# Optimization experiments

Hardware: AMD Instinct MI355X
Metric: run time of the kernel (lower is better)

The kernel has to match this reference:

```python
import jax, jax.numpy as jnp
import numpy as np
import math

B, S, H = 2, 2048, 2048
NH, HD = 32, 64
BASE, SCALE = 10000.0, 2.0
MAX_POS, ORIG_MAX_POS = 8192, 8192
BETA_FAST, BETA_SLOW = 32, 1
EPS = 1e-6


def _yarn_cos_sin():
    # revised_yarn: scale inv_freq by 1/((1-mask)*scale + mask)
    inv_freq = 1.0 / BASE ** (np.arange(0, HD, 2, dtype=np.float64) / HD)
    def corr(nr):
        return HD * math.log(ORIG_MAX_POS / (nr * 2 * math.pi)) / (2 * math.log(BASE))
    low = max(math.floor(corr(BETA_FAST)), 0)
    high = min(math.ceil(corr(BETA_SLOW)), HD - 1)
    hi = high + 0.001 if low == high else high
    ramp = np.clip((np.arange(HD // 2, dtype=np.float64) - low) / (hi - low), 0.0, 1.0)
    mask = 1.0 - ramp  # extrapolation_factor = 1
    inv_freq = inv_freq / ((1.0 - mask) * SCALE + mask)
    mscale = (0.1 * math.log(SCALE) + 1.0) if SCALE > 1 else 1.0
    t = np.arange(MAX_POS, dtype=np.float64)
    freqs = np.outer(t, inv_freq)
    emb = np.concatenate([freqs, freqs], axis=-1)
    return np.cos(emb) * mscale, np.sin(emb) * mscale

_COS_NP, _SIN_NP = _yarn_cos_sin()


def rotate_half(x):
    x1, x2 = jnp.split(x, 2, axis=-1)
    return jnp.concatenate([-x2, x1], axis=-1)


def rms_norm(x, w):
    v = jnp.mean(jnp.square(x.astype(jnp.float32)), axis=-1, keepdims=True)
    return (x.astype(jnp.float32) * jax.lax.rsqrt(v + EPS)).astype(x.dtype) * w


def localized_filtering(x, lf1, lf2, w1, b1, w2, b2, ln_w):
    # x: (B,S,H); torch works in (B,H,S,1) with kernel-(2,1) convs over seq
    residual = x
    xi = jnp.transpose(x, (0, 2, 1))[:, :, :, None]  # (B,H,S,1)
    xi = jnp.concatenate([lf1, xi], axis=2)          # (B,H,S+1,1)
    dn = ('NCHW', 'OIHW', 'NCHW')
    o1 = jax.lax.conv_general_dilated(xi, w1, (1, 1), 'VALID', dimension_numbers=dn)
    o1 = o1 + b1[None, :, None, None]                # (B,H/2,S,1)
    o1c = jnp.concatenate([lf2, o1], axis=2)         # (B,H/2,S+1,1)
    o2 = jax.lax.conv_general_dilated(o1c, w2, (1, 1), 'VALID', dimension_numbers=dn)
    o2 = o2 + b2[None, :, None, None]                # (B,H,S,1)
    o2 = jnp.transpose(o2[:, :, :, 0], (0, 2, 1))    # (B,S,H)
    return rms_norm(o2 + residual, ln_w)


def setup_inputs():
    key = jax.random.key(0)
    ks = jax.random.split(key, 8)
    f = lambda k, shp: jax.random.normal(k, shp, dtype=jnp.float32) * 0.02
    return {
        'hidden_states': jax.random.normal(ks[0], (B, S, H), dtype=jnp.float32),
        'position_ids': jnp.broadcast_to(jnp.arange(S, dtype=jnp.int32)[None, :], (B, S)),
        'lf1_cache': jnp.zeros((B, H, 1, 1), jnp.float32),
        'lf2_cache': jnp.zeros((B, H // 2, 1, 1), jnp.float32),
        'Wqk': f(ks[1], (2 * H, H)),
        'Wv': f(ks[2], (H, H)),
        'Wo': f(ks[3], (H, H)),
        'conv1_w': f(ks[4], (H // 2, H, 2, 1)),
        'conv1_b': jnp.zeros((H // 2,), jnp.float32),
        'conv2_w': f(ks[5], (H, H // 2, 2, 1)),
        'conv2_b': jnp.zeros((H,), jnp.float32),
        'ln_w': jnp.ones((H,), jnp.float32),
    }


def reference(hidden_states, position_ids, lf1_cache, lf2_cache, Wqk, Wv, Wo,
              conv1_w, conv1_b, conv2_w, conv2_b, ln_w):
    cos = jnp.asarray(_COS_NP, jnp.float32)
    sin = jnp.asarray(_SIN_NP, jnp.float32)
    # v from raw hidden states
    v = (hidden_states @ Wv.T).reshape(B, S, NH, HD).transpose(0, 2, 1, 3)  # (B,NH,S,HD)
    # localized filtering gate feeds q/k projection
    lf = localized_filtering(hidden_states, lf1_cache, lf2_cache,
                             conv1_w, conv1_b, conv2_w, conv2_b, ln_w)
    qk = (lf @ Wqk.T).reshape(B, S, NH, 2 * HD)  # per-head [q|k] split
    q = qk[..., :HD].transpose(0, 2, 1, 3)       # (B,NH,S,HD)
    k = qk[..., HD:].transpose(0, 2, 1, 3)
    cos_p = cos[position_ids][:, None, :, :]     # (B,1,S,HD)
    sin_p = sin[position_ids][:, None, :, :]
    q = q * cos_p + rotate_half(q) * sin_p
    k = k * cos_p + rotate_half(k) * sin_p
    scores = jnp.einsum('bhqd,bhkd->bhqk', q, k) / math.sqrt(HD)
    causal = jnp.tril(jnp.ones((S, S), dtype=bool))
    scores = jnp.where(causal[None, None], scores, jnp.finfo(scores.dtype).min)
    attn = jax.nn.softmax(scores, axis=-1)
    ctx = jnp.einsum('bhqk,bhkd->bhqd', attn, v)
    out = ctx.transpose(0, 2, 1, 3).reshape(B, S, H) @ Wo.T
    return out
```

## Files before the change

kernel.cpp:

```cpp
#include <hip/hip_runtime.h>
#include <hip/hip_bf16.h>
#include <math.h>
#include <stdint.h>

typedef __hip_bfloat16 bf16;
using f32x4 = __attribute__((ext_vector_type(4))) float;
using s16x8 = __attribute__((ext_vector_type(8))) short;

constexpr int Bc = 2, Sc = 2048, Hc = 2048, NHc = 32, HDc = 64;
constexpr int Mc = Bc * Sc;
constexpr int MAXPOS = 8192;

constexpr size_t OFF_WV  = 0;
constexpr size_t OFF_WQK = OFF_WV  + (size_t)Hc * Hc * 2;
constexpr size_t OFF_WO  = OFF_WQK + (size_t)2 * Hc * Hc * 2;
constexpr size_t OFF_W1  = OFF_WO  + (size_t)Hc * Hc * 2;
constexpr size_t OFF_W2  = OFF_W1  + (size_t)(Hc/2) * (2*Hc) * 2;
constexpr size_t OFF_HS  = OFF_W2  + (size_t)Hc * Hc * 2;
constexpr size_t OFF_XPR = OFF_HS  + (size_t)Mc * Hc * 2;
constexpr size_t OFF_O1  = OFF_XPR + (size_t)Mc * Hc * 2;
constexpr size_t OFF_O1P = OFF_O1  + (size_t)Mc * (Hc/2) * 2;
constexpr size_t OFF_O2  = OFF_O1P + (size_t)Mc * (Hc/2) * 2;
constexpr size_t OFF_LF  = OFF_O2  + (size_t)Mc * Hc * 4;
constexpr size_t OFF_VT  = OFF_LF  + (size_t)Mc * Hc * 2;
constexpr size_t OFF_COS = OFF_VT  + (size_t)Mc * Hc * 2;
constexpr size_t OFF_SIN = OFF_COS + (size_t)MAXPOS * HDc * 4;
constexpr size_t OFF_Q   = OFF_XPR;
constexpr size_t OFF_K   = OFF_HS;
constexpr size_t OFF_CTX = OFF_O1;

__device__ __forceinline__ f32x4 mfma16(s16x8 a, s16x8 b, f32x4 c) {
  return __builtin_amdgcn_mfma_f32_16x16x32_bf16(a, b, c, 0, 0, 0);
}
__device__ __forceinline__ void gload16(const bf16* g, bf16* l) {
  __builtin_amdgcn_global_load_lds(
      (__attribute__((address_space(1))) void*)g,
      (__attribute__((address_space(3))) void*)l, 16, 0, 0);
}
__device__ __forceinline__ uint16_t bfbits(float x) {
  union { bf16 h; uint16_t u; } v; v.h = __float2bfloat16(x); return v.u;
}
__device__ __forceinline__ uint32_t pkbf(float a, float b) {
  return (uint32_t)bfbits(a) | ((uint32_t)bfbits(b) << 16);
}
__device__ __forceinline__ void block_bar() {
  asm volatile("" ::: "memory");
  __builtin_amdgcn_s_barrier();
  asm volatile("" ::: "memory");
}
template <int N> __device__ __forceinline__ void vm_wait() {
  if constexpr (N == 0)      asm volatile("s_waitcnt vmcnt(0)" ::: "memory");
  else if constexpr (N == 3) asm volatile("s_waitcnt vmcnt(3)" ::: "memory");
  else if constexpr (N == 4) asm volatile("s_waitcnt vmcnt(4)" ::: "memory");
  else if constexpr (N == 6) asm volatile("s_waitcnt vmcnt(6)" ::: "memory");
  else if constexpr (N == 8) asm volatile("s_waitcnt vmcnt(8)" ::: "memory");
}

__global__ void k_cvt(const float* __restrict__ in, bf16* __restrict__ out, int n) {
  int i = blockIdx.x * 256 + threadIdx.x;
  if (i < n) out[i] = __float2bfloat16(in[i]);
}

__global__ void k_cvt_hs(const float* __restrict__ hs, const float* __restrict__ lf1,
                         bf16* __restrict__ hsb, bf16* __restrict__ xprev) {
  int i = blockIdx.x * 256 + threadIdx.x;
  if (i >= Mc * Hc) return;
  float v = hs[i];
  bf16 b = __float2bfloat16(v);
  hsb[i] = b;
  int row = i >> 11, col = i & (Hc - 1);
  int s = row & (Sc - 1), bb = row >> 11;
  if (s + 1 < Sc) xprev[i + Hc] = b;
  if (s == 0)     xprev[i] = __float2bfloat16(lf1[bb * Hc + col]);
}

__global__ void k_repack1(const float* __restrict__ w, bf16* __restrict__ out) {
  int i = blockIdx.x * 256 + threadIdx.x;
  if (i >= (Hc/2) * 2 * Hc) return;
  int oc = i >> 12, k = i & 4095;
  int ic = k & (Hc - 1), t = k >> 11;
  out[i] = __float2bfloat16(w[((size_t)oc * Hc + ic) * 2 + t]);
}
__global__ void k_repack2(const float* __restrict__ w, bf16* __restrict__ out) {
  int i = blockIdx.x * 256 + threadIdx.x;
  if (i >= Hc * Hc) return;
  int c = i >> 11, k = i & (Hc - 1);
  int oc = k & (Hc/2 - 1), t = k >> 10;
  out[i] = __float2bfloat16(w[((size_t)c * (Hc/2) + oc) * 2 + t]);
}

__global__ void k_prefill_o1p(const float* __restrict__ lf2, bf16* __restrict__ o1p) {
  int i = blockIdx.x * 256 + threadIdx.x;
  if (i >= Bc * (Hc/2)) return;
  int b = i >> 10, n = i & (Hc/2 - 1);
  o1p[(size_t)b * Sc * (Hc/2) + n] = __float2bfloat16(lf2[i]);
}

struct InvF { double v[32]; double mscale; };

__global__ void k_costab(InvF f, float* __restrict__ ct, float* __restrict__ st) {
  int i = blockIdx.x * 256 + threadIdx.x;
  if (i >= MAXPOS * HDc) return;
  int p = i >> 6, d = i & 63;
  double ang = (double)p * f.v[d & 31];
  ct[i] = (float)(cos(ang) * f.mscale);
  st[i] = (float)(sin(ang) * f.mscale);
}

__global__ __launch_bounds__(256) void k_rmsnorm(const float* __restrict__ x,
                                                 const float* __restrict__ w,
                                                 bf16* __restrict__ out) {
  __shared__ float red[4];
  int row = blockIdx.x;
  const float* xr = x + (size_t)row * Hc;
  float ss = 0.f;
  for (int c = threadIdx.x; c < Hc; c += 256) { float v = xr[c]; ss += v * v; }
  for (int off = 32; off; off >>= 1) ss += __shfl_down(ss, off, 64);
  if ((threadIdx.x & 63) == 0) red[threadIdx.x >> 6] = ss;
  __syncthreads();
  float sc = rsqrtf((red[0] + red[1] + red[2] + red[3]) / Hc + 1e-6f);
  for (int c = threadIdx.x; c < Hc; c += 256)
    out[(size_t)row * Hc + c] = __float2bfloat16(xr[c] * sc * w[c]);
}

template <int EPI, int BM = 128>
__global__ __launch_bounds__(256) void gemm_bt(
    const bf16* __restrict__ A0, const bf16* __restrict__ A1, int Ksplit,
    const bf16* __restrict__ Bw, int K, int N, void* __restrict__ Cout,
    const float* __restrict__ bias, const float* __restrict__ resid,
    bf16* __restrict__ aux) {
  constexpr int MR = BM / 32;
  __shared__ __align__(16) bf16 As[2][BM * 32];
  __shared__ __align__(16) bf16 Bs[2][128 * 32];
  const int tid = threadIdx.x;
  const int bm = blockIdx.y, bn = blockIdx.x;
  const int w = tid >> 6, l = tid & 63;
  const int wm = (w >> 1) * (BM / 2), wn = (w & 1) * 64;
  const int lrow = l & 15, lg = l >> 4, lk = lg * 8;
  const int r0 = tid >> 2, cofs = (tid & 3) * 8;

  auto stage = [&](int buf, int kt) {
    const int kcol = kt * 32;
    const bf16* Au; int kc;
    if (kcol < Ksplit) { Au = A0; kc = kcol; } else { Au = A1; kc = kcol - Ksplit; }
    gload16(Au + (size_t)(bm * BM + r0) * Ksplit + kc + cofs,        &As[buf][tid * 8]);
    if constexpr (BM == 128)
      gload16(Au + (size_t)(bm * BM + r0 + 64) * Ksplit + kc + cofs, &As[buf][2048 + tid * 8]);
    gload16(Bw + (size_t)(bn * 128 + r0) * K + kcol + cofs,          &Bs[buf][tid * 8]);
    gload16(Bw + (size_t)(bn * 128 + r0 + 64) * K + kcol + cofs,     &Bs[buf][2048 + tid * 8]);
  };

  f32x4 acc[MR][4] = {};
  const int nkt = K / 32;
  stage(0, 0);
  __syncthreads();
  for (int kt = 0; kt < nkt; ++kt) {
    const int cur = kt & 1;
    if (kt + 1 < nkt) stage(cur ^ 1, kt + 1);
    s16x8 af[MR], bfr[4];
#pragma unroll
    for (int m = 0; m < MR; ++m)
      af[m] = *(const s16x8*)&As[cur][(wm + m * 16 + lrow) * 32 + lk];
#pragma unroll
    for (int n = 0; n < 4; ++n)
      bfr[n] = *(const s16x8*)&Bs[cur][(wn + n * 16 + lrow) * 32 + lk];
    __builtin_amdgcn_s_setprio(1);
#pragma unroll
    for (int m = 0; m < MR; ++m)
#pragma unroll
      for (int n = 0; n < 4; ++n)
        acc[m][n] = mfma16(af[m], bfr[n], acc[m][n]);
    __builtin_amdgcn_s_setprio(0);
    __syncthreads();
  }
#pragma unroll
  for (int m = 0; m < MR; ++m)
#pragma unroll
    for (int n = 0; n < 4; ++n)
#pragma unroll
      for (int r = 0; r < 4; ++r) {
        const int grow = bm * BM + wm + m * 16 + lg * 4 + r;
        const int gcol = bn * 128 + wn + n * 16 + lrow;
        float v = acc[m][n][r];
        if constexpr (EPI == 1) {
          v += bias[gcol];
          bf16 bv = __float2bfloat16(v);
          ((bf16*)Cout)[(size_t)grow * N + gcol] = bv;
          if ((grow & (Sc - 1)) != Sc - 1) aux[(size_t)(grow + 1) * N + gcol] = bv;
        } else {
          ((float*)Cout)[(size_t)grow * N + gcol] = v;
        }
      }
}

template <int EPI, int BN>
__global__ __launch_bounds__(512, 2) void gemm8(
    const bf16* __restrict__ A0, const bf16* __restrict__ A1, int Ksplit,
    const bf16* __restrict__ Bw, int K, int N, void* __restrict__ Cout,
    const float* __restrict__ bias, const float* __restrict__ resid,
    const int* __restrict__ pos, const float* __restrict__ ct,
    const float* __restrict__ st, bf16* __restrict__ out2) {
  constexpr int BM = 256;
  constexpr int L = (BN == 256) ? 4 : 3;
  constexpr int TILE = (BM + BN) * 32;
  constexpr int MR = (BN == 256) ? 8 : 4;
  __shared__ __align__(16) bf16 lds[3][TILE];
  const int tid = threadIdx.x;
  const int w = tid >> 6, l = tid & 63;
  const int lrow = l & 15, lg = l >> 4;
  const int wm = (BN == 256) ? (w >> 2) * 128 : (w & 3) * 64;
  const int wn = (BN == 256) ? (w & 3) * 64 : (w >> 2) * 64;
  const int gx = gridDim.x;
  const int lin = blockIdx.y * gx + blockIdx.x;
  const int cx = gx >> 2, cy = gridDim.y >> 1;
  const int c = lin & 7, idx = lin >> 3;
  const int bn = (c & 3) * cx + idx % cx;
  const int bm = (c >> 2) * cy + idx / cx;

  auto ld1 = [&](const bf16* srcbase, size_t stride, bf16* ldst, int ci) {
    const int pr = ci >> 3, rem = ci & 7;
    const int r = pr * 2 + (rem >> 2), g = (rem & 3) ^ (pr & 3);
    gload16(srcbase + (size_t)r * stride + g * 8, ldst + ci * 8);
  };
  auto stage = [&](int kt, int slot) {
    const int kcol = kt * 32;
    const bf16* Au; int kc;
    if (kcol < Ksplit) { Au = A0; kc = kcol; } else { Au = A1; kc = kcol - Ksplit; }
    const bf16* As_ = Au + (size_t)bm * BM * Ksplit + kc;
    bf16* ldsA = lds[slot];
    ld1(As_, Ksplit, ldsA, tid);
    ld1(As_, Ksplit, ldsA, tid + 512);
    const bf16* Bs_ = Bw + (size_t)bn * BN * K + kcol;
    bf16* ldsB = lds[slot] + BM * 32;
    ld1(Bs_, K, ldsB, tid);
    if constexpr (BN == 256) ld1(Bs_, K, ldsB, tid + 512);
  };
  auto frag = [&](const bf16* base, int r) -> s16x8 {
    const int s = ((r >> 1) << 3) + ((r & 1) << 2) + (lg ^ ((r >> 1) & 3));
    return *(const s16x8*)(base + s * 8);
  };

  f32x4 acc[MR][4] = {};
  const int nkt = K / 32;
  stage(0, 0);
  stage(1, 1);
  for (int t = 0; t < nkt; ++t) {
    if (t + 2 < nkt) { stage(t + 2, (t + 2) % 3); vm_wait<2 * L>(); }
    else if (t + 1 < nkt) { vm_wait<L>(); }
    else { vm_wait<0>(); }
    block_bar();
    const bf16* Asl = lds[t % 3];
    const bf16* Bsl = Asl + BM * 32;
    s16x8 af[MR], bfr[4];
#pragma unroll
    for (int m = 0; m < MR; ++m) af[m] = frag(Asl, wm + m * 16 + lrow);
#pragma unroll
    for (int n = 0; n < 4; ++n) bfr[n] = frag(Bsl, wn + n * 16 + lrow);
    __builtin_amdgcn_s_setprio(1);
#pragma unroll
    for (int m = 0; m < MR; ++m)
#pragma unroll
      for (int n = 0; n < 4; ++n)
        acc[m][n] = mfma16(af[m], bfr[n], acc[m][n]);
    __builtin_amdgcn_s_setprio(0);
    block_bar();
  }
  if constexpr (EPI == 6) {
    const int gcol0 = bn * BN + wn;
    const int h = gcol0 >> 7, half = (gcol0 >> 6) & 1;
    bf16* outp = half ? out2 : (bf16*)Cout;
    const float qsc = half ? 1.0f : 0.125f * 1.44269504088896f;
#pragma unroll
    for (int m = 0; m < MR; ++m)
#pragma unroll
      for (int r = 0; r < 4; ++r) {
        const int grow = bm * BM + wm + m * 16 + lg * 4 + r;
        const int p = pos[grow];
        const int bb = grow >> 11, s = grow & (Sc - 1);
        bf16* rowp = outp + ((size_t)(bb * NHc + h) * Sc + s) * 64;
#pragma unroll
        for (int n = 0; n < 2; ++n) {
          const int dd = n * 16 + lrow;
          const float c0 = ct[p * 64 + dd],      s0 = st[p * 64 + dd];
          const float c1 = ct[p * 64 + 32 + dd], s1 = st[p * 64 + 32 + dd];
          const float v0 = acc[m][n][r], v1 = acc[m][n + 2][r];
          rowp[dd]      = __float2bfloat16((v0 * c0 - v1 * s0) * qsc);
          rowp[dd + 32] = __float2bfloat16((v1 * c1 + v0 * s1) * qsc);
        }
      }
  } else {
#pragma unroll
    for (int m = 0; m < MR; ++m)
#pragma unroll
      for (int n = 0; n < 4; ++n)
#pragma unroll
        for (int r = 0; r < 4; ++r) {
          const int grow = bm * BM + wm + m * 16 + lg * 4 + r;
          const int gcol = bn * BN + wn + n * 16 + lrow;
          float v = acc[m][n][r];
          if constexpr (EPI == 2) {
            v += bias[gcol] + resid[(size_t)grow * N + gcol];
            ((float*)Cout)[(size_t)grow * N + gcol] = v;
          } else if constexpr (EPI == 5) {
            const int b = gcol >> 11, s = gcol & (Sc - 1);
            ((bf16*)Cout)[((size_t)(b * Hc + grow)) * Sc + s] = __float2bfloat16(v);
          } else {
            ((float*)Cout)[(size_t)grow * N + gcol] = v;
          }
        }
  }
}

__global__ __launch_bounds__(256) void k_attn(const bf16* __restrict__ Q,
                                              const bf16* __restrict__ Kg,
                                              const bf16* __restrict__ Vt,
                                              bf16* __restrict__ ctx) {
  __shared__ __align__(16) bf16 Ks[2][64 * 64];
  __shared__ __align__(16) bf16 Vs[2][64 * 64];
  __shared__ __align__(16) uint32_t Pl[4][2][2][16][20];
  const int tid = threadIdx.x;
  const int w = tid >> 6, l = tid & 63;
  const int lrow = l & 15, lg = l >> 4, lk = lg * 8;
  const int bh = blockIdx.x;
  const int tile = blockIdx.y;
  const bf16* Qp = Q  + (size_t)bh * Sc * HDc;
  const bf16* Kp = Kg + (size_t)bh * Sc * HDc;
  const bf16* Vp = Vt + (size_t)bh * HDc * Sc;
  const int b = bh >> 5, h = bh & 31;
  const s16x8 ones8 = {16256, 16256, 16256, 16256, 16256, 16256, 16256, 16256};

  const int srow0 = tid >> 3, schunk = tid & 7;

  for (int pass = 0; pass < 2; ++pass) {
    const int base = (pass == 0) ? tile * 128 : (Sc - 128 - tile * 128);
    const int q0 = base + w * 32;
    const int NT = base / 64 + 2;

    s16x8 qa[2][2];
#pragma unroll
    for (int m = 0; m < 2; ++m)
#pragma unroll
      for (int hf = 0; hf < 2; ++hf)
        qa[m][hf] = *(const s16x8*)&Qp[(size_t)(q0 + m * 16 + lrow) * 64 + hf * 32 + lk];

    f32x4 o[2][4] = {};
    f32x4 lsf[2] = {};
    float mx[2] = {-1e30f, -1e30f};

    {
      gload16(Kp + (size_t)srow0 * 64 + ((schunk ^ (srow0 & 7)) << 3), &Ks[0][tid * 8]);
      gload16(Kp + (size_t)(32 + srow0) * 64 + ((schunk ^ ((32 + srow0) & 7)) << 3),
              &Ks[0][2048 + tid * 8]);
      gload16(Vp + (size_t)srow0 * Sc + ((schunk ^ (srow0 & 7)) << 3), &Vs[0][tid * 8]);
      gload16(Vp + (size_t)(32 + srow0) * Sc + ((schunk ^ ((32 + srow0) & 7)) << 3),
              &Vs[0][2048 + tid * 8]);
    }
    __syncthreads();

    for (int t = 0; t < NT; ++t) {
      const int cur = t & 1;
      const int kv0 = t * 64;
      if (t + 1 < NT) {
        const int nkv = kv0 + 64;
        const int nb = cur ^ 1;
        gload16(Kp + (size_t)(nkv + srow0) * 64 + ((schunk ^ (srow0 & 7)) << 3),
                &Ks[nb][tid * 8]);
        gload16(Kp + (size_t)(nkv + 32 + srow0) * 64 + ((schunk ^ ((32 + srow0) & 7)) << 3),
                &Ks[nb][2048 + tid * 8]);
        gload16(Vp + (size_t)srow0 * Sc + nkv + ((schunk ^ (srow0 & 7)) << 3),
                &Vs[nb][tid * 8]);
        gload16(Vp + (size_t)(32 + srow0) * Sc + nkv + ((schunk ^ ((32 + srow0) & 7)) << 3),
                &Vs[nb][2048 + tid * 8]);
      }
      if (kv0 <= q0) {
        s16x8 kc[8], vc[4][2];
#pragma unroll
        for (int c = 0; c < 4; ++c)
#pragma unroll
          for (int hf = 0; hf < 2; ++hf) {
            const int row = c * 16 + lrow;
            kc[c * 2 + hf] =
                *(const s16x8*)&Ks[cur][row * 64 + (((hf << 2) + lg) ^ (row & 7)) * 8];
          }
#pragma unroll
        for (int db = 0; db < 4; ++db)
#pragma unroll
          for (int kh = 0; kh < 2; ++kh) {
            const int row = db * 16 + lrow;
            vc[db][kh] =
                *(const s16x8*)&Vs[cur][row * 64 + (((kh << 2) + lg) ^ (row & 7)) * 8];
          }
        const bool lastit = (kv0 + 64 > q0);

#pragma unroll
        for (int m = 0; m < 2; ++m) {
          f32x4 s[4];
          __builtin_amdgcn_s_setprio(1);
#pragma unroll
          for (int c = 0; c < 4; ++c) {
            f32x4 z = {};
            z = mfma16(kc[c * 2], qa[m][0], z);
            z = mfma16(kc[c * 2 + 1], qa[m][1], z);
            s[c] = z;
          }
          __builtin_amdgcn_s_setprio(0);

          if (lastit) {
            const int qq = q0 + m * 16 + lrow;
#pragma unroll
            for (int c = 0; c < 4; ++c)
#pragma unroll
              for (int r = 0; r < 4; ++r)
                if (kv0 + c * 16 + lg * 4 + r > qq) s[c][r] = -1e30f;
          }
          float t16 = fmaxf(
              fmaxf(fmaxf(fmaxf(s[0][0], s[0][1]), fmaxf(s[0][2], s[0][3])),
                    fmaxf(fmaxf(s[1][0], s[1][1]), fmaxf(s[1][2], s[1][3]))),
              fmaxf(fmaxf(fmaxf(s[2][0], s[2][1]), fmaxf(s[2][2], s[2][3])),
                    fmaxf(fmaxf(s[3][0], s[3][1]), fmaxf(s[3][2], s[3][3]))));
          if (!__all(t16 <= mx[m] + 8.0f)) {
            t16 = fmaxf(t16, __shfl_xor(t16, 16, 64));
            t16 = fmaxf(t16, __shfl_xor(t16, 32, 64));
            const float mnew = fmaxf(mx[m], t16);
            const float sold = __builtin_amdgcn_exp2f(mx[m] - mnew);
            mx[m] = mnew;
            lsf[m] *= sold;
#pragma unroll
            for (int db = 0; db < 4; ++db) o[m][db] *= sold;
          }
          float p[4][4];
#pragma unroll
          for (int c = 0; c < 4; ++c)
#pragma unroll
            for (int r = 0; r < 4; ++r)
              p[c][r] = __builtin_amdgcn_exp2f(s[c][r] - mx[m]);
#pragma unroll
          for (int kh = 0; kh < 2; ++kh) {
            *(uint64_t*)&Pl[w][m][kh][lrow][lg * 2] =
                (uint64_t)pkbf(p[kh * 2][0], p[kh * 2][1]) |
                ((uint64_t)pkbf(p[kh * 2][2], p[kh * 2][3]) << 32);
            *(uint64_t*)&Pl[w][m][kh][lrow][8 + lg * 2] =
                (uint64_t)pkbf(p[kh * 2 + 1][0], p[kh * 2 + 1][1]) |
                ((uint64_t)pkbf(p[kh * 2 + 1][2], p[kh * 2 + 1][3]) << 32);
          }
          const s16x8 pb0 = *(const s16x8*)&Pl[w][m][0][lrow][lg * 4];
          const s16x8 pb1 = *(const s16x8*)&Pl[w][m][1][lrow][lg * 4];
          __builtin_amdgcn_s_setprio(1);
#pragma unroll
          for (int db = 0; db < 4; ++db) o[m][db] = mfma16(vc[db][0], pb0, o[m][db]);
          lsf[m] = mfma16(ones8, pb0, lsf[m]);
#pragma unroll
          for (int db = 0; db < 4; ++db) o[m][db] = mfma16(vc[db][1], pb1, o[m][db]);
          lsf[m] = mfma16(ones8, pb1, lsf[m]);
          __builtin_amdgcn_s_setprio(0);
        }
      }
      __syncthreads();
    }
#pragma unroll
    for (int m = 0; m < 2; ++m) {
      const float inv = 1.0f / lsf[m][0];
      const int qrow = q0 + m * 16 + lrow;
      const size_t rowoff = ((size_t)(b * Sc + qrow)) * Hc + h * 64;
#pragma unroll
      for (int db = 0; db < 4; ++db) {
        uint64_t pk = (uint64_t)bfbits(o[m][db][0] * inv) |
                      ((uint64_t)bfbits(o[m][db][1] * inv) << 16) |
                      ((uint64_t)bfbits(o[m][db][2] * inv) << 32) |
                      ((uint64_t)bfbits(o[m][db][3] * inv) << 48);
        *(uint64_t*)&ctx[rowoff + db * 16 + lg * 4] = pk;
      }
    }
    __syncthreads();
  }
}

extern "C" void kernel_launch(void* const* d_in, const int* in_sizes, int n_in,
                              void* d_out, int out_size, void* d_ws, size_t ws_size,
                              hipStream_t stream) {
  (void)in_sizes; (void)n_in; (void)out_size; (void)ws_size;
  const float* hs  = (const float*)d_in[0];
  const int*   pos = (const int*)d_in[1];
  const float* lf1 = (const float*)d_in[2];
  const float* lf2 = (const float*)d_in[3];
  const float* Wqk = (const float*)d_in[4];
  const float* Wv  = (const float*)d_in[5];
  const float* Wo  = (const float*)d_in[6];
  const float* c1w = (const float*)d_in[7];
  const float* c1b = (const float*)d_in[8];
  const float* c2w = (const float*)d_in[9];
  const float* c2b = (const float*)d_in[10];
  const float* lnw = (const float*)d_in[11];
  float* out = (float*)d_out;
  char*  ws  = (char*)d_ws;

  bf16* wvB   = (bf16*)(ws + OFF_WV);
  bf16* wqkB  = (bf16*)(ws + OFF_WQK);
  bf16* woB   = (bf16*)(ws + OFF_WO);
  bf16* w1B   = (bf16*)(ws + OFF_W1);
  bf16* w2B   = (bf16*)(ws + OFF_W2);
  bf16* hsB   = (bf16*)(ws + OFF_HS);
  bf16* xprB  = (bf16*)(ws + OFF_XPR);
  bf16* o1B   = (bf16*)(ws + OFF_O1);
  bf16* o1pB  = (bf16*)(ws + OFF_O1P);
  float* o2F  = (float*)(ws + OFF_O2);
  bf16* lfB   = (bf16*)(ws + OFF_LF);
  bf16* vtB   = (bf16*)(ws + OFF_VT);
  float* cosT = (float*)(ws + OFF_COS);
  float* sinT = (float*)(ws + OFF_SIN);
  bf16* qB    = (bf16*)(ws + OFF_Q);
  bf16* kB    = (bf16*)(ws + OFF_K);
  bf16* ctxB  = (bf16*)(ws + OFF_CTX);

  InvF f;
  {
    const double base = 10000.0, scale = 2.0;
    const int hd = HDc;
    auto corr = [&](double nr) {
      return hd * log(8192.0 / (nr * 2.0 * M_PI)) / (2.0 * log(base));
    };
    double low = floor(corr(32.0)); if (low < 0) low = 0;
    double high = ceil(corr(1.0));  if (high > hd - 1) high = hd - 1;
    double hi = (low == high) ? high + 0.001 : high;
    for (int i = 0; i < 32; ++i) {
      double inv = 1.0 / pow(base, (2.0 * i) / hd);
      double ramp = ((double)i - low) / (hi - low);
      ramp = ramp < 0.0 ? 0.0 : (ramp > 1.0 ? 1.0 : ramp);
      double mask = 1.0 - ramp;
      f.v[i] = inv / ((1.0 - mask) * scale + mask);
    }
    f.mscale = 0.1 * log(scale) + 1.0;
  }

  k_cvt<<<(Hc * Hc + 255) / 256, 256, 0, stream>>>(Wv, wvB, Hc * Hc);
  k_cvt<<<(2 * Hc * Hc + 255) / 256, 256, 0, stream>>>(Wqk, wqkB, 2 * Hc * Hc);
  k_cvt<<<(Hc * Hc + 255) / 256, 256, 0, stream>>>(Wo, woB, Hc * Hc);
  k_repack1<<<((Hc / 2) * 2 * Hc + 255) / 256, 256, 0, stream>>>(c1w, w1B);
  k_repack2<<<(Hc * Hc + 255) / 256, 256, 0, stream>>>(c2w, w2B);
  k_cvt_hs<<<(Mc * Hc + 255) / 256, 256, 0, stream>>>(hs, lf1, hsB, xprB);
  k_prefill_o1p<<<(Bc * (Hc / 2) + 255) / 256, 256, 0, stream>>>(lf2, o1pB);
  k_costab<<<(MAXPOS * HDc + 255) / 256, 256, 0, stream>>>(f, cosT, sinT);

  gemm_bt<1, 64><<<dim3((Hc / 2) / 128, Mc / 64), 256, 0, stream>>>(
      xprB, hsB, Hc, w1B, 2 * Hc, Hc / 2, o1B, c1b, nullptr, o1pB);
  gemm8<5, 128><<<dim3(Mc / 128, Hc / 256), 512, 0, stream>>>(
      wvB, wvB, Hc, hsB, Hc, Mc, vtB, nullptr, nullptr, nullptr, nullptr, nullptr, nullptr);
  gemm8<2, 128><<<dim3(Hc / 128, Mc / 256), 512, 0, stream>>>(
      o1pB, o1B, Hc / 2, w2B, Hc, Hc, o2F, c2b, hs, nullptr, nullptr, nullptr, nullptr);
  k_rmsnorm<<<Mc, 256, 0, stream>>>(o2F, lnw, lfB);
  gemm8<6, 256><<<dim3((2 * Hc) / 256, Mc / 256), 512, 0, stream>>>(
      lfB, lfB, Hc, wqkB, Hc, 2 * Hc, qB, nullptr, nullptr, pos, cosT, sinT, kB);
  k_attn<<<dim3(64, 8), 256, 0, stream>>>(qB, kB, vtB, ctxB);
  gemm8<4, 128><<<dim3(Hc / 128, Mc / 256), 512, 0, stream>>>(
      ctxB, ctxB, Hc, woB, Hc, Hc, out, nullptr, nullptr, nullptr, nullptr, nullptr, nullptr);
}
```

Baseline: 461.6 us.

## Port conv1 GEMM to gemm8 and split attention passes across 512-thread blocks

The conv1 GEMM moves from the older double-buffered 256-thread gemm_bt kernel to the triple-buffered 512-thread gemm8 kernel with a new 128x128 tile variant and a bias/shifted-copy epilogue. The attention kernel now runs its two causal query passes (early and late tiles) concurrently in two 4-wave halves of a 512-thread block, instead of looping over them one after another. This is meant to balance the causal work within each block and add more waves per block to hide latency. In exchange it adds LDS for the per-wave P buffers and a launch-bounds hint that limits register use.

```diff
diff --git a/kernel.cpp b/kernel.cpp
--- a/kernel.cpp
+++ b/kernel.cpp
@@ -50,6 +50,7 @@
 }
 template <int N> __device__ __forceinline__ void vm_wait() {
   if constexpr (N == 0)      asm volatile("s_waitcnt vmcnt(0)" ::: "memory");
+  else if constexpr (N == 2) asm volatile("s_waitcnt vmcnt(2)" ::: "memory");
   else if constexpr (N == 3) asm volatile("s_waitcnt vmcnt(3)" ::: "memory");
   else if constexpr (N == 4) asm volatile("s_waitcnt vmcnt(4)" ::: "memory");
   else if constexpr (N == 6) asm volatile("s_waitcnt vmcnt(6)" ::: "memory");
@@ -123,93 +124,25 @@
     out[(size_t)row * Hc + c] = __float2bfloat16(xr[c] * sc * w[c]);
 }
 
-template <int EPI, int BM = 128>
-__global__ __launch_bounds__(256) void gemm_bt(
-    const bf16* __restrict__ A0, const bf16* __restrict__ A1, int Ksplit,
-    const bf16* __restrict__ Bw, int K, int N, void* __restrict__ Cout,
-    const float* __restrict__ bias, const float* __restrict__ resid,
-    bf16* __restrict__ aux) {
-  constexpr int MR = BM / 32;
-  __shared__ __align__(16) bf16 As[2][BM * 32];
-  __shared__ __align__(16) bf16 Bs[2][128 * 32];
-  const int tid = threadIdx.x;
-  const int bm = blockIdx.y, bn = blockIdx.x;
-  const int w = tid >> 6, l = tid & 63;
-  const int wm = (w >> 1) * (BM / 2), wn = (w & 1) * 64;
-  const int lrow = l & 15, lg = l >> 4, lk = lg * 8;
-  const int r0 = tid >> 2, cofs = (tid & 3) * 8;
-
-  auto stage = [&](int buf, int kt) {
-    const int kcol = kt * 32;
-    const bf16* Au; int kc;
-    if (kcol < Ksplit) { Au = A0; kc = kcol; } else { Au = A1; kc = kcol - Ksplit; }
-    gload16(Au + (size_t)(bm * BM + r0) * Ksplit + kc + cofs,        &As[buf][tid * 8]);
-    if constexpr (BM == 128)
-      gload16(Au + (size_t)(bm * BM + r0 + 64) * Ksplit + kc + cofs, &As[buf][2048 + tid * 8]);
-    gload16(Bw + (size_t)(bn * 128 + r0) * K + kcol + cofs,          &Bs[buf][tid * 8]);
-    gload16(Bw + (size_t)(bn * 128 + r0 + 64) * K + kcol + cofs,     &Bs[buf][2048 + tid * 8]);
-  };
-
-  f32x4 acc[MR][4] = {};
-  const int nkt = K / 32;
-  stage(0, 0);
-  __syncthreads();
-  for (int kt = 0; kt < nkt; ++kt) {
-    const int cur = kt & 1;
-    if (kt + 1 < nkt) stage(cur ^ 1, kt + 1);
-    s16x8 af[MR], bfr[4];
-#pragma unroll
-    for (int m = 0; m < MR; ++m)
-      af[m] = *(const s16x8*)&As[cur][(wm + m * 16 + lrow) * 32 + lk];
-#pragma unroll
-    for (int n = 0; n < 4; ++n)
-      bfr[n] = *(const s16x8*)&Bs[cur][(wn + n * 16 + lrow) * 32 + lk];
-    __builtin_amdgcn_s_setprio(1);
-#pragma unroll
-    for (int m = 0; m < MR; ++m)
-#pragma unroll
-      for (int n = 0; n < 4; ++n)
-        acc[m][n] = mfma16(af[m], bfr[n], acc[m][n]);
-    __builtin_amdgcn_s_setprio(0);
-    __syncthreads();
-  }
-#pragma unroll
-  for (int m = 0; m < MR; ++m)
-#pragma unroll
-    for (int n = 0; n < 4; ++n)
-#pragma unroll
-      for (int r = 0; r < 4; ++r) {
-        const int grow = bm * BM + wm + m * 16 + lg * 4 + r;
-        const int gcol = bn * 128 + wn + n * 16 + lrow;
-        float v = acc[m][n][r];
-        if constexpr (EPI == 1) {
-          v += bias[gcol];
-          bf16 bv = __float2bfloat16(v);
-          ((bf16*)Cout)[(size_t)grow * N + gcol] = bv;
-          if ((grow & (Sc - 1)) != Sc - 1) aux[(size_t)(grow + 1) * N + gcol] = bv;
-        } else {
-          ((float*)Cout)[(size_t)grow * N + gcol] = v;
-        }
-      }
-}
-
-template <int EPI, int BN>
+template <int EPI, int BM, int BN>
 __global__ __launch_bounds__(512, 2) void gemm8(
     const bf16* __restrict__ A0, const bf16* __restrict__ A1, int Ksplit,
     const bf16* __restrict__ Bw, int K, int N, void* __restrict__ Cout,
     const float* __restrict__ bias, const float* __restrict__ resid,
     const int* __restrict__ pos, const float* __restrict__ ct,
     const float* __restrict__ st, bf16* __restrict__ out2) {
-  constexpr int BM = 256;
-  constexpr int L = (BN == 256) ? 4 : 3;
+  constexpr int L = (BM + BN) / 128;
   constexpr int TILE = (BM + BN) * 32;
-  constexpr int MR = (BN == 256) ? 8 : 4;
+  constexpr int MF = (BM == 256) ? ((BN == 256) ? 8 : 4) : 4;
+  constexpr int NF = (BN == 256) ? 4 : ((BM == 256) ? 4 : 2);
   __shared__ __align__(16) bf16 lds[3][TILE];
   const int tid = threadIdx.x;
   const int w = tid >> 6, l = tid & 63;
   const int lrow = l & 15, lg = l >> 4;
-  const int wm = (BN == 256) ? (w >> 2) * 128 : (w & 3) * 64;
-  const int wn = (BN == 256) ? (w & 3) * 64 : (w >> 2) * 64;
+  const int wm = (BM == 256) ? ((BN == 256) ? (w >> 2) * 128 : (w & 3) * 64)
+                             : (w >> 2) * 64;
+  const int wn = (BM == 256) ? ((BN == 256) ? (w & 3) * 64 : (w >> 2) * 64)
+                             : (w & 3) * 32;
   const int gx = gridDim.x;
   const int lin = blockIdx.y * gx + blockIdx.x;
   const int cx = gx >> 2, cy = gridDim.y >> 1;
@@ -229,7 +162,7 @@
     const bf16* As_ = Au + (size_t)bm * BM * Ksplit + kc;
     bf16* ldsA = lds[slot];
     ld1(As_, Ksplit, ldsA, tid);
-    ld1(As_, Ksplit, ldsA, tid + 512);
+    if constexpr (BM == 256) ld1(As_, Ksplit, ldsA, tid + 512);
     const bf16* Bs_ = Bw + (size_t)bn * BN * K + kcol;
     bf16* ldsB = lds[slot] + BM * 32;
     ld1(Bs_, K, ldsB, tid);
@@ -240,7 +173,7 @@
     return *(const s16x8*)(base + s * 8);
   };
 
-  f32x4 acc[MR][4] = {};
+  f32x4 acc[MF][NF] = {};
   const int nkt = K / 32;
   stage(0, 0);
   stage(1, 1);
@@ -251,16 +184,16 @@
     block_bar();
     const bf16* Asl = lds[t % 3];
     const bf16* Bsl = Asl + BM * 32;
-    s16x8 af[MR], bfr[4];
-#pragma unroll
-    for (int m = 0; m < MR; ++m) af[m] = frag(Asl, wm + m * 16 + lrow);
-#pragma unroll
-    for (int n = 0; n < 4; ++n) bfr[n] = frag(Bsl, wn + n * 16 + lrow);
+    s16x8 af[MF], bfr[NF];
+#pragma unroll
+    for (int m = 0; m < MF; ++m) af[m] = frag(Asl, wm + m * 16 + lrow);
+#pragma unroll
+    for (int n = 0; n < NF; ++n) bfr[n] = frag(Bsl, wn + n * 16 + lrow);
     __builtin_amdgcn_s_setprio(1);
 #pragma unroll
-    for (int m = 0; m < MR; ++m)
-#pragma unroll
-      for (int n = 0; n < 4; ++n)
+    for (int m = 0; m < MF; ++m)
+#pragma unroll
+      for (int n = 0; n < NF; ++n)
         acc[m][n] = mfma16(af[m], bfr[n], acc[m][n]);
     __builtin_amdgcn_s_setprio(0);
     block_bar();
@@ -271,7 +204,7 @@
     bf16* outp = half ? out2 : (bf16*)Cout;
     const float qsc = half ? 1.0f : 0.125f * 1.44269504088896f;
 #pragma unroll
-    for (int m = 0; m < MR; ++m)
+    for (int m = 0; m < MF; ++m)
 #pragma unroll
       for (int r = 0; r < 4; ++r) {
         const int grow = bm * BM + wm + m * 16 + lg * 4 + r;
@@ -290,15 +223,20 @@
       }
   } else {
 #pragma unroll
-    for (int m = 0; m < MR; ++m)
-#pragma unroll
-      for (int n = 0; n < 4; ++n)
+    for (int m = 0; m < MF; ++m)
+#pragma unroll
+      for (int n = 0; n < NF; ++n)
 #pragma unroll
         for (int r = 0; r < 4; ++r) {
           const int grow = bm * BM + wm + m * 16 + lg * 4 + r;
           const int gcol = bn * BN + wn + n * 16 + lrow;
           float v = acc[m][n][r];
-          if constexpr (EPI == 2) {
+          if constexpr (EPI == 1) {
+            v += bias[gcol];
+            bf16 bv = __float2bfloat16(v);
+            ((bf16*)Cout)[(size_t)grow * N + gcol] = bv;
+            if ((grow & (Sc - 1)) != Sc - 1) out2[(size_t)(grow + 1) * N + gcol] = bv;
+          } else if constexpr (EPI == 2) {
             v += bias[gcol] + resid[(size_t)grow * N + gcol];
             ((float*)Cout)[(size_t)grow * N + gcol] = v;
           } else if constexpr (EPI == 5) {
@@ -311,13 +249,13 @@
   }
 }
 
-__global__ __launch_bounds__(256) void k_attn(const bf16* __restrict__ Q,
-                                              const bf16* __restrict__ Kg,
-                                              const bf16* __restrict__ Vt,
-                                              bf16* __restrict__ ctx) {
+__global__ __launch_bounds__(512, 4) void k_attn(const bf16* __restrict__ Q,
+                                                 const bf16* __restrict__ Kg,
+                                                 const bf16* __restrict__ Vt,
+                                                 bf16* __restrict__ ctx) {
   __shared__ __align__(16) bf16 Ks[2][64 * 64];
   __shared__ __align__(16) bf16 Vs[2][64 * 64];
-  __shared__ __align__(16) uint32_t Pl[4][2][2][16][20];
+  __shared__ __align__(16) uint32_t Pl[8][2][2][16][20];
   const int tid = threadIdx.x;
   const int w = tid >> 6, l = tid & 63;
   const int lrow = l & 15, lg = l >> 4, lk = lg * 8;
@@ -329,149 +267,136 @@
   const int b = bh >> 5, h = bh & 31;
   const s16x8 ones8 = {16256, 16256, 16256, 16256, 16256, 16256, 16256, 16256};
 
+  const int set = w >> 2, ws = w & 3;
+  const int base = (set == 0) ? tile * 128 : (Sc - 128 - tile * 128);
+  const int q0 = base + ws * 32;
+  const int NT = 32 - 2 * tile;
+
   const int srow0 = tid >> 3, schunk = tid & 7;
 
-  for (int pass = 0; pass < 2; ++pass) {
-    const int base = (pass == 0) ? tile * 128 : (Sc - 128 - tile * 128);
-    const int q0 = base + w * 32;
-    const int NT = base / 64 + 2;
-
-    s16x8 qa[2][2];
-#pragma unroll
-    for (int m = 0; m < 2; ++m)
-#pragma unroll
-      for (int hf = 0; hf < 2; ++hf)
-        qa[m][hf] = *(const s16x8*)&Qp[(size_t)(q0 + m * 16 + lrow) * 64 + hf * 32 + lk];
-
-    f32x4 o[2][4] = {};
-    f32x4 lsf[2] = {};
-    float mx[2] = {-1e30f, -1e30f};
-
-    {
-      gload16(Kp + (size_t)srow0 * 64 + ((schunk ^ (srow0 & 7)) << 3), &Ks[0][tid * 8]);
-      gload16(Kp + (size_t)(32 + srow0) * 64 + ((schunk ^ ((32 + srow0) & 7)) << 3),
-              &Ks[0][2048 + tid * 8]);
-      gload16(Vp + (size_t)srow0 * Sc + ((schunk ^ (srow0 & 7)) << 3), &Vs[0][tid * 8]);
-      gload16(Vp + (size_t)(32 + srow0) * Sc + ((schunk ^ ((32 + srow0) & 7)) << 3),
-              &Vs[0][2048 + tid * 8]);
-    }
-    __syncthreads();
-
-    for (int t = 0; t < NT; ++t) {
-      const int cur = t & 1;
-      const int kv0 = t * 64;
-      if (t + 1 < NT) {
-        const int nkv = kv0 + 64;
-        const int nb = cur ^ 1;
-        gload16(Kp + (size_t)(nkv + srow0) * 64 + ((schunk ^ (srow0 & 7)) << 3),
-                &Ks[nb][tid * 8]);
-        gload16(Kp + (size_t)(nkv + 32 + srow0) * 64 + ((schunk ^ ((32 + srow0) & 7)) << 3),
-                &Ks[nb][2048 + tid * 8]);
-        gload16(Vp + (size_t)srow0 * Sc + nkv + ((schunk ^ (srow0 & 7)) << 3),
-                &Vs[nb][tid * 8]);
-        gload16(Vp + (size_t)(32 + srow0) * Sc + nkv + ((schunk ^ ((32 + srow0) & 7)) << 3),
-                &Vs[nb][2048 + tid * 8]);
-      }
-      if (kv0 <= q0) {
-        s16x8 kc[8], vc[4][2];
+  auto stage = [&](int kv0, int buf) {
+    gload16(Kp + (size_t)(kv0 + srow0) * 64 + ((schunk ^ (srow0 & 7)) << 3),
+            &Ks[buf][tid * 8]);
+    gload16(Vp + (size_t)srow0 * Sc + kv0 + ((schunk ^ (srow0 & 7)) << 3),
+            &Vs[buf][tid * 8]);
+  };
+
+  s16x8 qa[2][2];
+#pragma unroll
+  for (int m = 0; m < 2; ++m)
+#pragma unroll
+    for (int hf = 0; hf < 2; ++hf)
+      qa[m][hf] = *(const s16x8*)&Qp[(size_t)(q0 + m * 16 + lrow) * 64 + hf * 32 + lk];
+
+  f32x4 o[2][4] = {};
+  f32x4 lsf[2] = {};
+  float mx[2] = {-1e30f, -1e30f};
+
+  stage(0, 0);
+  __syncthreads();
+
+  for (int t = 0; t < NT; ++t) {
+    const int cur = t & 1;
+    const int kv0 = t * 64;
+    if (t + 1 < NT) stage(kv0 + 64, cur ^ 1);
+    if (kv0 <= q0) {
+      s16x8 kc[8], vc[4][2];
+#pragma unroll
+      for (int c = 0; c < 4; ++c)
+#pragma unroll
+        for (int hf = 0; hf < 2; ++hf) {
+          const int row = c * 16 + lrow;
+          kc[c * 2 + hf] =
+              *(const s16x8*)&Ks[cur][row * 64 + (((hf << 2) + lg) ^ (row & 7)) * 8];
+        }
+#pragma unroll
+      for (int db = 0; db < 4; ++db)
+#pragma unroll
+        for (int kh = 0; kh < 2; ++kh) {
+          const int row = db * 16 + lrow;
+          vc[db][kh] =
+              *(const s16x8*)&Vs[cur][row * 64 + (((kh << 2) + lg) ^ (row & 7)) * 8];
+        }
+      const bool lastit = (kv0 + 64 > q0);
+
+#pragma unroll
+      for (int m = 0; m < 2; ++m) {
+        f32x4 s[4];
+        __builtin_amdgcn_s_setprio(1);
+#pragma unroll
+        for (int c = 0; c < 4; ++c) {
+          f32x4 z = {};
+          z = mfma16(kc[c * 2], qa[m][0], z);
+          z = mfma16(kc[c * 2 + 1], qa[m][1], z);
+          s[c] = z;
+        }
+        __builtin_amdgcn_s_setprio(0);
+
+        if (lastit) {
+          const int qq = q0 + m * 16 + lrow;
+#pragma unroll
+          for (int c = 0; c < 4; ++c)
+#pragma unroll
+            for (int r = 0; r < 4; ++r)
+              if (kv0 + c * 16 + lg * 4 + r > qq) s[c][r] = -1e30f;
+        }
+        float t16 = fmaxf(
+            fmaxf(fmaxf(fmaxf(s[0][0], s[0][1]), fmaxf(s[0][2], s[0][3])),
+                  fmaxf(fmaxf(s[1][0], s[1][1]), fmaxf(s[1][2], s[1][3]))),
+            fmaxf(fmaxf(fmaxf(s[2][0], s[2][1]), fmaxf(s[2][2], s[2][3])),
+                  fmaxf(fmaxf(s[3][0], s[3][1]), fmaxf(s[3][2], s[3][3]))));
+        if (!__all(t16 <= mx[m] + 8.0f)) {
+          t16 = fmaxf(t16, __shfl_xor(t16, 16, 64));
+          t16 = fmaxf(t16, __shfl_xor(t16, 32, 64));
+          const float mnew = fmaxf(mx[m], t16);
+          const float sold = __builtin_amdgcn_exp2f(mx[m] - mnew);
+          mx[m] = mnew;
+          lsf[m] *= sold;
+#pragma unroll
+          for (int db = 0; db < 4; ++db) o[m][db] *= sold;
+        }
+        float p[4][4];
 #pragma unroll
         for (int c = 0; c < 4; ++c)
 #pragma unroll
-          for (int hf = 0; hf < 2; ++hf) {
-            const int row = c * 16 + lrow;
-            kc[c * 2 + hf] =
-                *(const s16x8*)&Ks[cur][row * 64 + (((hf << 2) + lg) ^ (row & 7)) * 8];
-          }
-#pragma unroll
-        for (int db = 0; db < 4; ++db)
-#pragma unroll
-          for (int kh = 0; kh < 2; ++kh) {
-            const int row = db * 16 + lrow;
-            vc[db][kh] =
-                *(const s16x8*)&Vs[cur][row * 64 + (((kh << 2) + lg) ^ (row & 7)) * 8];
-          }
-        const bool lastit = (kv0 + 64 > q0);
-
-#pragma unroll
-        for (int m = 0; m < 2; ++m) {
-          f32x4 s[4];
-          __builtin_amdgcn_s_setprio(1);
-#pragma unroll
-          for (int c = 0; c < 4; ++c) {
-            f32x4 z = {};
-            z = mfma16(kc[c * 2], qa[m][0], z);
-            z = mfma16(kc[c * 2 + 1], qa[m][1], z);
-            s[c] = z;
-          }
-          __builtin_amdgcn_s_setprio(0);
-
-          if (lastit) {
-            const int qq = q0 + m * 16 + lrow;
-#pragma unroll
-            for (int c = 0; c < 4; ++c)
-#pragma unroll
-              for (int r = 0; r < 4; ++r)
-                if (kv0 + c * 16 + lg * 4 + r > qq) s[c][r] = -1e30f;
-          }
-          float t16 = fmaxf(
-              fmaxf(fmaxf(fmaxf(s[0][0], s[0][1]), fmaxf(s[0][2], s[0][3])),
-                    fmaxf(fmaxf(s[1][0], s[1][1]), fmaxf(s[1][2], s[1][3]))),
-              fmaxf(fmaxf(fmaxf(s[2][0], s[2][1]), fmaxf(s[2][2], s[2][3])),
-                    fmaxf(fmaxf(s[3][0], s[3][1]), fmaxf(s[3][2], s[3][3]))));
-          if (!__all(t16 <= mx[m] + 8.0f)) {
-            t16 = fmaxf(t16, __shfl_xor(t16, 16, 64));
-            t16 = fmaxf(t16, __shfl_xor(t16, 32, 64));
-            const float mnew = fmaxf(mx[m], t16);
-            const float sold = __builtin_amdgcn_exp2f(mx[m] - mnew);
-            mx[m] = mnew;
-            lsf[m] *= sold;
-#pragma unroll
-            for (int db = 0; db < 4; ++db) o[m][db] *= sold;
-          }
-          float p[4][4];
-#pragma unroll
-          for (int c = 0; c < 4; ++c)
-#pragma unroll
-            for (int r = 0; r < 4; ++r)
-              p[c][r] = __builtin_amdgcn_exp2f(s[c][r] - mx[m]);
-#pragma unroll
-          for (int kh = 0; kh < 2; ++kh) {
-            *(uint64_t*)&Pl[w][m][kh][lrow][lg * 2] =
-                (uint64_t)pkbf(p[kh * 2][0], p[kh * 2][1]) |
-                ((uint64_t)pkbf(p[kh * 2][2], p[kh * 2][3]) << 32);
-            *(uint64_t*)&Pl[w][m][kh][lrow][8 + lg * 2] =
-                (uint64_t)pkbf(p[kh * 2 + 1][0], p[kh * 2 + 1][1]) |
-                ((uint64_t)pkbf(p[kh * 2 + 1][2], p[kh * 2 + 1][3]) << 32);
-          }
-          const s16x8 pb0 = *(const s16x8*)&Pl[w][m][0][lrow][lg * 4];
-          const s16x8 pb1 = *(const s16x8*)&Pl[w][m][1][lrow][lg * 4];
-          __builtin_amdgcn_s_setprio(1);
-#pragma unroll
-          for (int db = 0; db < 4; ++db) o[m][db] = mfma16(vc[db][0], pb0, o[m][db]);
-          lsf[m] = mfma16(ones8, pb0, lsf[m]);
-#pragma unroll
-          for (int db = 0; db < 4; ++db) o[m][db] = mfma16(vc[db][1], pb1, o[m][db]);
-          lsf[m] = mfma16(ones8, pb1, lsf[m]);
-          __builtin_amdgcn_s_setprio(0);
-        }
-      }
-      __syncthreads();
-    }
-#pragma unroll
-    for (int m = 0; m < 2; ++m) {
-      const float inv = 1.0f / lsf[m][0];
-      const int qrow = q0 + m * 16 + lrow;
-      const size_t rowoff = ((size_t)(b * Sc + qrow)) * Hc + h * 64;
-#pragma unroll
-      for (int db = 0; db < 4; ++db) {
-        uint64_t pk = (uint64_t)bfbits(o[m][db][0] * inv) |
-                      ((uint64_t)bfbits(o[m][db][1] * inv) << 16) |
-                      ((uint64_t)bfbits(o[m][db][2] * inv) << 32) |
-                      ((uint64_t)bfbits(o[m][db][3] * inv) << 48);
-        *(uint64_t*)&ctx[rowoff + db * 16 + lg * 4] = pk;
+          for (int r = 0; r < 4; ++r)
+            p[c][r] = __builtin_amdgcn_exp2f(s[c][r] - mx[m]);
+#pragma unroll
+        for (int kh = 0; kh < 2; ++kh) {
+          *(uint64_t*)&Pl[w][m][kh][lrow][lg * 2] =
+              (uint64_t)pkbf(p[kh * 2][0], p[kh * 2][1]) |
+              ((uint64_t)pkbf(p[kh * 2][2], p[kh * 2][3]) << 32);
+          *(uint64_t*)&Pl[w][m][kh][lrow][8 + lg * 2] =
+              (uint64_t)pkbf(p[kh * 2 + 1][0], p[kh * 2 + 1][1]) |
+              ((uint64_t)pkbf(p[kh * 2 + 1][2], p[kh * 2 + 1][3]) << 32);
+        }
+        const s16x8 pb0 = *(const s16x8*)&Pl[w][m][0][lrow][lg * 4];
+        const s16x8 pb1 = *(const s16x8*)&Pl[w][m][1][lrow][lg * 4];
+        __builtin_amdgcn_s_setprio(1);
+#pragma unroll
+        for (int db = 0; db < 4; ++db) o[m][db] = mfma16(vc[db][0], pb0, o[m][db]);
+        lsf[m] = mfma16(ones8, pb0, lsf[m]);
+#pragma unroll
+        for (int db = 0; db < 4; ++db) o[m][db] = mfma16(vc[db][1], pb1, o[m][db]);
+        lsf[m] = mfma16(ones8, pb1, lsf[m]);
+        __builtin_amdgcn_s_setprio(0);
       }
     }
     __syncthreads();
+  }
+#pragma unroll
+  for (int m = 0; m < 2; ++m) {
+    const float inv = 1.0f / lsf[m][0];
+    const int qrow = q0 + m * 16 + lrow;
+    const size_t rowoff = ((size_t)(b * Sc + qrow)) * Hc + h * 64;
+#pragma unroll
+    for (int db = 0; db < 4; ++db) {
+      uint64_t pk = (uint64_t)bfbits(o[m][db][0] * inv) |
+                    ((uint64_t)bfbits(o[m][db][1] * inv) << 16) |
+                    ((uint64_t)bfbits(o[m][db][2] * inv) << 32) |
+                    ((uint64_t)bfbits(o[m][db][3] * inv) << 48);
+      *(uint64_t*)&ctx[rowoff + db * 16 + lg * 4] = pk;
+    }
   }
 }
 
@@ -541,16 +466,17 @@
   k_prefill_o1p<<<(Bc * (Hc / 2) + 255) / 256, 256, 0, stream>>>(lf2, o1pB);
   k_costab<<<(MAXPOS * HDc + 255) / 256, 256, 0, stream>>>(f, cosT, sinT);
 
-  gemm_bt<1, 64><<<dim3((Hc / 2) / 128, Mc / 64), 256, 0, stream>>>(
-      xprB, hsB, Hc, w1B, 2 * Hc, Hc / 2, o1B, c1b, nullptr, o1pB);
-  gemm8<5, 128><<<dim3(Mc / 128, Hc / 256), 512, 0, stream>>>(
+  gemm8<1, 128, 128><<<dim3((Hc / 2) / 128, Mc / 128), 512, 0, stream>>>(
+      xprB, hsB, Hc, w1B, 2 * Hc, Hc / 2, o1B, c1b, nullptr,
+      nullptr, nullptr, nullptr, o1pB);
+  gemm8<5, 256, 128><<<dim3(Mc / 128, Hc / 256), 512, 0, stream>>>(
       wvB, wvB, Hc, hsB, Hc, Mc, vtB, nullptr, nullptr, nullptr, nullptr, nullptr, nullptr);
-  gemm8<2, 128><<<dim3(Hc / 128, Mc / 256), 512, 0, stream>>>(
+  gemm8<2, 256, 128><<<dim3(Hc / 128, Mc / 256), 512, 0, stream>>>(
       o1pB, o1B, Hc / 2, w2B, Hc, Hc, o2F, c2b, hs, nullptr, nullptr, nullptr, nullptr);
   k_rmsnorm<<<Mc, 256, 0, stream>>>(o2F, lnw, lfB);
-  gemm8<6, 256><<<dim3((2 * Hc) / 256, Mc / 256), 512, 0, stream>>>(
+  gemm8<6, 256, 256><<<dim3((2 * Hc) / 256, Mc / 256), 512, 0, stream>>>(
       lfB, lfB, Hc, wqkB, Hc, 2 * Hc, qB, nullptr, nullptr, pos, cosT, sinT, kB);
-  k_attn<<<dim3(64, 8), 256, 0, stream>>>(qB, kB, vtB, ctxB);
-  gemm8<4, 128><<<dim3(Hc / 128, Mc / 256), 512, 0, stream>>>(
+  k_attn<<<dim3(64, 8), 512, 0, stream>>>(qB, kB, vtB, ctxB);
+  gemm8<4, 256, 128><<<dim3(Hc / 128, Mc / 256), 512, 0, stream>>>(
       ctxB, ctxB, Hc, woB, Hc, Hc, out, nullptr, nullptr, nullptr, nullptr, nullptr, nullptr);
 }
```

New measurement: 565.2 us. +22.4%, slower.
